# Kernel optimization log

Hardware: AMD Instinct MI355X
Metric: run time of the kernel (lower is better)

The kernel has to match this reference:

```python
import jax, jax.numpy as jnp
import numpy as np

IN_CH = 256
BOT = IN_CH // 2  # bottleneck channels
B, W, H = 4, 64, 64


def setup_inputs() -> dict:
    key = jax.random.key(0)
    ks = jax.random.split(key, 10)
    s_in = 1.0 / np.sqrt(IN_CH)   # torch Conv2d default init scale (kaiming-ish bound)
    s_bt = 1.0 / np.sqrt(BOT)
    return {
        "X": jax.random.normal(ks[0], (B, IN_CH, W, H), dtype=jnp.float32),
        "Wq": jax.random.uniform(ks[1], (BOT, IN_CH), jnp.float32, -s_in, s_in),
        "bq": jax.random.uniform(ks[2], (BOT,), jnp.float32, -s_in, s_in),
        "Wk": jax.random.uniform(ks[3], (BOT, IN_CH), jnp.float32, -s_in, s_in),
        "bk": jax.random.uniform(ks[4], (BOT,), jnp.float32, -s_in, s_in),
        "Wv": jax.random.uniform(ks[5], (BOT, IN_CH), jnp.float32, -s_in, s_in),
        "bv": jax.random.uniform(ks[6], (BOT,), jnp.float32, -s_in, s_in),
        "Wo": jax.random.uniform(ks[7], (IN_CH, BOT), jnp.float32, -s_bt, s_bt),
        "bo": jax.random.uniform(ks[8], (IN_CH,), jnp.float32, -s_bt, s_bt),
        "gamma": 0.1 * jax.random.normal(ks[9], (1,), dtype=jnp.float32),
    }


def reference(X, Wq, bq, Wk, bk, Wv, bv, Wo, bo, gamma):
    b, c, w, h = X.shape
    n = w * h
    Xf = X.reshape(b, c, n)  # [b, c, n] — 1x1 conv == per-pixel linear
    q = jnp.einsum('oc,bcn->bon', Wq, Xf) + bq[None, :, None]  # [b, c/2, n]
    k = jnp.einsum('oc,bcn->bon', Wk, Xf) + bk[None, :, None]
    v = jnp.einsum('oc,bcn->bon', Wv, Xf) + bv[None, :, None]
    # score[b,i,j] = sum_c q[b,c,i] * k[b,c,j]; softmax over dim=1 (query index i)
    score = jnp.einsum('bci,bcj->bij', q, k)          # [b, n, n]
    attn = jax.nn.softmax(score, axis=1)
    out = jnp.einsum('bci,bij->bcj', v, attn)         # [b, c/2, n]
    out = jnp.einsum('oc,bcn->bon', Wo, out) + bo[None, :, None]  # [b, c, n]
    out = out.reshape(b, c, w, h)
    return gamma[0] * out + X
```

## Files before the change

### kernel.cpp

```cpp
#include <hip/hip_runtime.h>
#include <math.h>

#define NBATCH 4
#define CIN    256
#define CBOT   128
#define NPIX   4096
#define NPART  4
#define LOG2E  1.44269504f

typedef __attribute__((ext_vector_type(4))) float f32x4;
typedef __attribute__((ext_vector_type(8))) short bf16x8;

__device__ __forceinline__ unsigned short f2bf(float f) {
    union { float f; unsigned u; } v; v.f = f;
    unsigned r = (v.u + 0x7FFFu + ((v.u >> 16) & 1u)) >> 16;
    return (unsigned short)r;
}
__device__ __forceinline__ unsigned pk2bf(float a, float b) {
#if __has_builtin(__builtin_amdgcn_cvt_pk_bf16_f32)
    auto r = __builtin_amdgcn_cvt_pk_bf16_f32(a, b);
    unsigned u; __builtin_memcpy(&u, &r, 4); return u;
#else
    return (unsigned)f2bf(a) | ((unsigned)f2bf(b) << 16);
#endif
}
__device__ __forceinline__ float fexp2(float x) {
#if __has_builtin(__builtin_amdgcn_exp2f)
    return __builtin_amdgcn_exp2f(x);
#else
    return exp2f(x);
#endif
}
__device__ __forceinline__ void plswap32(unsigned &a, unsigned &b) {
#if __has_builtin(__builtin_amdgcn_permlane32_swap)
    auto r = __builtin_amdgcn_permlane32_swap(a, b, false, false);
    a = (unsigned)r[0]; b = (unsigned)r[1];
#else
    asm volatile("v_permlane32_swap_b32 %0, %1" : "+v"(a), "+v"(b));
#endif
}
__device__ __forceinline__ void plswap16(unsigned &a, unsigned &b) {
#if __has_builtin(__builtin_amdgcn_permlane16_swap)
    auto r = __builtin_amdgcn_permlane16_swap(a, b, false, false);
    a = (unsigned)r[0]; b = (unsigned)r[1];
#else
    asm volatile("v_permlane16_swap_b32 %0, %1" : "+v"(a), "+v"(b));
#endif
}

__global__ __launch_bounds__(256) void k_wcvt(
    const float* __restrict__ Wq, const float* __restrict__ Wk,
    const float* __restrict__ Wv, const float* __restrict__ Wo,
    unsigned short* __restrict__ Wb)
{
    const int f4 = (blockIdx.x * 256 + threadIdx.x) * 4;
    const int reg = f4 >> 15, loc = f4 & 32767;
    const float* __restrict__ W = (reg == 0) ? Wq : (reg == 1) ? Wk : (reg == 2) ? Wv : Wo;
    const float sc = (reg == 1) ? LOG2E : 1.f;
    float4 v = *(const float4*)(W + loc);
    uint2 u;
    u.x = pk2bf(v.x * sc, v.y * sc);
    u.y = pk2bf(v.z * sc, v.w * sc);
    *(uint2*)&Wb[f4] = u;
}

__global__ __launch_bounds__(256) void k_qkvx(
    const float* __restrict__ X,
    const unsigned short* __restrict__ Wb,
    const float* __restrict__ bq, const float* __restrict__ bk,
    const float* __restrict__ bv,
    unsigned short* __restrict__ Qt, unsigned short* __restrict__ Kt,
    unsigned short* __restrict__ Vt)
{
    __shared__ __align__(16) unsigned short Xs[32][264];
    const int tid = threadIdx.x;
    const int wv = tid >> 6, lane = tid & 63;
    const int grp = lane & 15, quad = lane >> 4;
    const int pbase = blockIdx.x * 32;
    const int b     = blockIdx.y;
    const float* __restrict__ Xg = X + (size_t)b * CIN * NPIX + pbase;

#pragma unroll
    for (int k = 0; k < 8; ++k) {
        int f = tid + 256 * k;
        int c = f >> 3, pg = (f & 7) << 2;
        float4 v = *(const float4*)(Xg + (size_t)c * NPIX + pg);
        Xs[pg + 0][c] = f2bf(v.x);
        Xs[pg + 1][c] = f2bf(v.y);
        Xs[pg + 2][c] = f2bf(v.z);
        Xs[pg + 3][c] = f2bf(v.w);
    }
    __syncthreads();

    const unsigned short* __restrict__ Wqb = Wb;
    const unsigned short* __restrict__ Wkb = Wb + 32768;
    const unsigned short* __restrict__ Wvb = Wb + 65536;
    const int obase = 32 * wv;

    f32x4 aQ[2][2], aK[2][2], aV[2][2];
#pragma unroll
    for (int mt = 0; mt < 2; ++mt)
#pragma unroll
        for (int nt = 0; nt < 2; ++nt) {
            aQ[mt][nt] = (f32x4)0.f; aK[mt][nt] = (f32x4)0.f; aV[mt][nt] = (f32x4)0.f;
        }

    for (int ks = 0; ks < 8; ++ks) {
        bf16x8 bx[2];
#pragma unroll
        for (int nt = 0; nt < 2; ++nt)
            bx[nt] = *(const bf16x8*)&Xs[nt * 16 + grp][ks * 32 + quad * 8];
        bf16x8 wq_[2], wk_[2], wv_[2];
#pragma unroll
        for (int mt = 0; mt < 2; ++mt) {
            const size_t roff = (size_t)(obase + mt * 16 + grp) * CIN + ks * 32 + quad * 8;
            wq_[mt] = *(const bf16x8*)&Wqb[roff];
            wk_[mt] = *(const bf16x8*)&Wkb[roff];
            wv_[mt] = *(const bf16x8*)&Wvb[roff];
        }
#pragma unroll
        for (int mt = 0; mt < 2; ++mt)
#pragma unroll
            for (int nt = 0; nt < 2; ++nt) {
                aQ[mt][nt] = __builtin_amdgcn_mfma_f32_16x16x32_bf16(wq_[mt], bx[nt], aQ[mt][nt], 0, 0, 0);
                aK[mt][nt] = __builtin_amdgcn_mfma_f32_16x16x32_bf16(wk_[mt], bx[nt], aK[mt][nt], 0, 0, 0);
                aV[mt][nt] = __builtin_amdgcn_mfma_f32_16x16x32_bf16(bx[mt], wv_[nt], aV[mt][nt], 0, 0, 0);
            }
    }

    unsigned short* Qb_ = Qt + (size_t)b * NPIX * CBOT;
    unsigned short* Kb_ = Kt + (size_t)b * NPIX * CBOT;
#pragma unroll
    for (int mt = 0; mt < 2; ++mt) {
        int o0 = obase + mt * 16 + quad * 4;
        float b4q[4], b4k[4];
#pragma unroll
        for (int r = 0; r < 4; ++r) { b4q[r] = bq[o0 + r]; b4k[r] = bk[o0 + r] * LOG2E; }
#pragma unroll
        for (int nt = 0; nt < 2; ++nt) {
            int p = pbase + nt * 16 + grp;
            uint2 uq, uk;
            uq.x = pk2bf(aQ[mt][nt][0] + b4q[0], aQ[mt][nt][1] + b4q[1]);
            uq.y = pk2bf(aQ[mt][nt][2] + b4q[2], aQ[mt][nt][3] + b4q[3]);
            uk.x = pk2bf(aK[mt][nt][0] + b4k[0], aK[mt][nt][1] + b4k[1]);
            uk.y = pk2bf(aK[mt][nt][2] + b4k[2], aK[mt][nt][3] + b4k[3]);
            *(uint2*)&Qb_[(size_t)p * CBOT + o0] = uq;
            *(uint2*)&Kb_[(size_t)p * CBOT + o0] = uk;
        }
    }
    unsigned short* Vb_ = Vt + (size_t)b * CBOT * NPIX;
#pragma unroll
    for (int nt = 0; nt < 2; ++nt) {
        int o = obase + nt * 16 + grp;
        float bb = bv[o];
#pragma unroll
        for (int mt = 0; mt < 2; ++mt) {
            int p0 = pbase + mt * 16 + quad * 4;
            uint2 u;
            u.x = pk2bf(aV[mt][nt][0] + bb, aV[mt][nt][1] + bb);
            u.y = pk2bf(aV[mt][nt][2] + bb, aV[mt][nt][3] + bb);
            *(uint2*)&Vb_[(size_t)o * NPIX + p0] = u;
        }
    }
}

__global__ __launch_bounds__(256, 2) void k_flash(
    const unsigned short* __restrict__ Qt,
    const unsigned short* __restrict__ Kt,
    const unsigned short* __restrict__ Vt,
    unsigned short* __restrict__ Opart,
    float* __restrict__ Lpart)
{
    extern __shared__ __align__(16) unsigned short lds[];
#define QS(bi, r, c) lds[(bi) * 8704 + (r) * 136 + (c)]
#define VS(bi, r, c) lds[17408 + (bi) * 9216 + (r) * 72 + (c)]
    const int tid  = threadIdx.x;
    const int wv   = tid >> 6, lane = tid & 63;
    const int grp  = lane & 15, quad = lane >> 4;
    const int jblk = blockIdx.x * 128;
    const int part = blockIdx.y;
    const int b    = blockIdx.z;
    const int tbeg = part * (64 / NPART);
    const int tend = tbeg + (64 / NPART);
    const unsigned short* __restrict__ Qb = Qt + (size_t)b * NPIX * CBOT;
    const unsigned short* __restrict__ Kb = Kt + (size_t)b * NPIX * CBOT;
    const unsigned short* __restrict__ Vb = Vt + (size_t)b * CBOT * NPIX;

    bf16x8 bk[2][4];
#pragma unroll
    for (int nt = 0; nt < 2; ++nt)
#pragma unroll
        for (int ks = 0; ks < 4; ++ks)
            bk[nt][ks] = *(const bf16x8*)&Kb[
                (size_t)(jblk + wv * 32 + nt * 16 + grp) * CBOT + ks * 32 + quad * 8];

    bf16x8 aones;
#pragma unroll
    for (int t = 0; t < 8; ++t) aones[t] = (short)0x3F80;

    f32x4 o[8][2];
#pragma unroll
    for (int ct = 0; ct < 8; ++ct) { o[ct][0] = (f32x4)0.f; o[ct][1] = (f32x4)0.f; }
    f32x4 lacc[2] = {(f32x4)0.f, (f32x4)0.f};

    const int qrow = tid >> 4, qch = tid & 15;
    const int vrow = tid >> 3, vch = tid & 7;
    bf16x8 qreg[4], vreg[4];
#pragma unroll
    for (int k = 0; k < 4; ++k) {
        qreg[k] = *(const bf16x8*)&Qb[(size_t)(tbeg * 64 + qrow + 16 * k) * CBOT + qch * 8];
        vreg[k] = *(const bf16x8*)&Vb[(size_t)(vrow + 32 * k) * NPIX + tbeg * 64 + vch * 8];
    }
#pragma unroll
    for (int k = 0; k < 4; ++k) {
        *(bf16x8*)&QS(0, qrow + 16 * k, qch * 8) = qreg[k];
        *(bf16x8*)&VS(0, vrow + 32 * k, vch * 8) = vreg[k];
    }
    {
        const int i1 = (tbeg + 1) * 64;
#pragma unroll
        for (int k = 0; k < 4; ++k) {
            qreg[k] = *(const bf16x8*)&Qb[(size_t)(i1 + qrow + 16 * k) * CBOT + qch * 8];
            vreg[k] = *(const bf16x8*)&Vb[(size_t)(vrow + 32 * k) * NPIX + i1 + vch * 8];
        }
    }
    __syncthreads();

    for (int it = tbeg; it < tend; ++it) {
        const int cur = (it - tbeg) & 1;

        f32x4 sf[4][2];
#pragma unroll
        for (int mt = 0; mt < 4; ++mt) { sf[mt][0] = (f32x4)0.f; sf[mt][1] = (f32x4)0.f; }
#pragma unroll
        for (int mt = 0; mt < 4; ++mt)
#pragma unroll
            for (int ks = 0; ks < 4; ++ks) {
                bf16x8 aq_ = *(const bf16x8*)&QS(cur, mt * 16 + grp, ks * 32 + quad * 8);
                sf[mt][0] = __builtin_amdgcn_mfma_f32_16x16x32_bf16(aq_, bk[0][ks], sf[mt][0], 0, 0, 0);
                sf[mt][1] = __builtin_amdgcn_mfma_f32_16x16x32_bf16(aq_, bk[1][ks], sf[mt][1], 0, 0, 0);
            }

        if (it + 1 < tend) {
#pragma unroll
            for (int k = 0; k < 4; ++k) {
                *(bf16x8*)&QS(cur ^ 1, qrow + 16 * k, qch * 8) = qreg[k];
                *(bf16x8*)&VS(cur ^ 1, vrow + 32 * k, vch * 8) = vreg[k];
            }
            if (it + 2 < tend) {
                const int i2 = (it + 2) * 64;
#pragma unroll
                for (int k = 0; k < 4; ++k) {
                    qreg[k] = *(const bf16x8*)&Qb[(size_t)(i2 + qrow + 16 * k) * CBOT + qch * 8];
                    vreg[k] = *(const bf16x8*)&Vb[(size_t)(vrow + 32 * k) * NPIX + i2 + vch * 8];
                }
            }
        }

        bf16x8 pf[2][2];
#pragma unroll
        for (int nt = 0; nt < 2; ++nt)
#pragma unroll
            for (int h = 0; h < 2; ++h) {
                unsigned u0a = pk2bf(fexp2(sf[2 * h][nt][0]),     fexp2(sf[2 * h][nt][1]));
                unsigned u1a = pk2bf(fexp2(sf[2 * h][nt][2]),     fexp2(sf[2 * h][nt][3]));
                unsigned u0b = pk2bf(fexp2(sf[2 * h + 1][nt][0]), fexp2(sf[2 * h + 1][nt][1]));
                unsigned u1b = pk2bf(fexp2(sf[2 * h + 1][nt][2]), fexp2(sf[2 * h + 1][nt][3]));
                plswap32(u0a, u0b); plswap16(u0a, u0b);
                plswap32(u1a, u1b); plswap16(u1a, u1b);
                union { unsigned u[4]; bf16x8 v; } cvt;
                cvt.u[0] = u0a; cvt.u[1] = u1a; cvt.u[2] = u0b; cvt.u[3] = u1b;
                pf[nt][h] = cvt.v;
            }

#pragma unroll
        for (int ct = 0; ct < 8; ++ct)
#pragma unroll
            for (int h = 0; h < 2; ++h) {
                bf16x8 av_ = *(const bf16x8*)&VS(cur, ct * 16 + grp, h * 32 + quad * 8);
                o[ct][0] = __builtin_amdgcn_mfma_f32_16x16x32_bf16(av_, pf[0][h], o[ct][0], 0, 0, 0);
                o[ct][1] = __builtin_amdgcn_mfma_f32_16x16x32_bf16(av_, pf[1][h], o[ct][1], 0, 0, 0);
            }
#pragma unroll
        for (int nt = 0; nt < 2; ++nt) {
            lacc[nt] = __builtin_amdgcn_mfma_f32_16x16x32_bf16(aones, pf[nt][0], lacc[nt], 0, 0, 0);
            lacc[nt] = __builtin_amdgcn_mfma_f32_16x16x32_bf16(aones, pf[nt][1], lacc[nt], 0, 0, 0);
        }

        if (it + 1 < tend) __syncthreads();
    }

    unsigned short* Ob = Opart + ((size_t)(part * NBATCH + b) * NPIX + jblk) * CBOT;
#pragma unroll
    for (int nt = 0; nt < 2; ++nt) {
        const size_t jrow = (size_t)(wv * 32 + nt * 16 + grp) * CBOT;
#pragma unroll
        for (int ct = 0; ct < 8; ++ct) {
            uint2 u;
            u.x = pk2bf(o[ct][nt][0], o[ct][nt][1]);
            u.y = pk2bf(o[ct][nt][2], o[ct][nt][3]);
            *(uint2*)&Ob[jrow + ct * 16 + quad * 4] = u;
        }
    }
    if (quad == 0) {
#pragma unroll
        for (int nt = 0; nt < 2; ++nt)
            Lpart[(size_t)(part * NBATCH + b) * NPIX + jblk + wv * 32 + nt * 16 + grp] =
                lacc[nt][0];
    }
#undef QS
#undef VS
}

__global__ __launch_bounds__(256) void k_oproj(
    const unsigned short* __restrict__ Opart, const float* __restrict__ Lpart,
    const unsigned short* __restrict__ Wob, const float* __restrict__ bo,
    const float* __restrict__ gamma, const float* __restrict__ X,
    float* __restrict__ Out)
{
    const int tid = threadIdx.x;
    const int wv = tid >> 6, lane = tid & 63;
    const int grp = lane & 15, quad = lane >> 4;
    const int pbase = blockIdx.x * 32;
    const int b     = blockIdx.y;
    const int obase = 64 * wv;

    f32x4 acc[2][4];
#pragma unroll
    for (int mt = 0; mt < 2; ++mt)
#pragma unroll
        for (int nt = 0; nt < 4; ++nt) acc[mt][nt] = (f32x4)0.f;

    for (int ks = 0; ks < 4; ++ks) {
        bf16x8 bw[4];
#pragma unroll
        for (int nt = 0; nt < 4; ++nt)
            bw[nt] = *(const bf16x8*)&Wob[(size_t)(obase + nt * 16 + grp) * CBOT + ks * 32 + quad * 8];
#pragma unroll
        for (int mt = 0; mt < 2; ++mt) {
            int p = pbase + mt * 16 + grp;
#pragma unroll
            for (int part = 0; part < NPART; ++part) {
                bf16x8 ao = *(const bf16x8*)&Opart[
                    ((size_t)(part * NBATCH + b) * NPIX + p) * CBOT + ks * 32 + quad * 8];
#pragma unroll
                for (int nt = 0; nt < 4; ++nt)
                    acc[mt][nt] = __builtin_amdgcn_mfma_f32_16x16x32_bf16(ao, bw[nt], acc[mt][nt], 0, 0, 0);
            }
        }
    }

    float linv[2][4];
#pragma unroll
    for (int mt = 0; mt < 2; ++mt)
#pragma unroll
        for (int r = 0; r < 4; ++r) {
            int p = pbase + mt * 16 + quad * 4 + r;
            float ls = 0.f;
#pragma unroll
            for (int part = 0; part < NPART; ++part)
                ls += Lpart[(size_t)(part * NBATCH + b) * NPIX + p];
            linv[mt][r] = 1.f / ls;
        }
    float g = gamma[0];
#pragma unroll
    for (int nt = 0; nt < 4; ++nt) {
        int o = obase + nt * 16 + grp;
        float bb = bo[o];
#pragma unroll
        for (int mt = 0; mt < 2; ++mt) {
            int p0 = pbase + mt * 16 + quad * 4;
            size_t base = (size_t)b * CIN * NPIX + (size_t)o * NPIX + p0;
            float4 x4 = *(const float4*)(X + base);
            float4 r4;
            r4.x = g * (acc[mt][nt][0] * linv[mt][0] + bb) + x4.x;
            r4.y = g * (acc[mt][nt][1] * linv[mt][1] + bb) + x4.y;
            r4.z = g * (acc[mt][nt][2] * linv[mt][2] + bb) + x4.z;
            r4.w = g * (acc[mt][nt][3] * linv[mt][3] + bb) + x4.w;
            *(float4*)(Out + base) = r4;
        }
    }
}

extern "C" void kernel_launch(void* const* d_in, const int* in_sizes, int n_in,
                              void* d_out, int out_size, void* d_ws, size_t ws_size,
                              hipStream_t stream)
{
    (void)in_sizes; (void)n_in; (void)out_size; (void)ws_size;
    const float* X     = (const float*)d_in[0];
    const float* Wq    = (const float*)d_in[1];
    const float* bq    = (const float*)d_in[2];
    const float* Wk    = (const float*)d_in[3];
    const float* bk    = (const float*)d_in[4];
    const float* Wv    = (const float*)d_in[5];
    const float* bv    = (const float*)d_in[6];
    const float* Wo    = (const float*)d_in[7];
    const float* bo    = (const float*)d_in[8];
    const float* gamma = (const float*)d_in[9];
    float* out = (float*)d_out;

    const size_t BNC = (size_t)NBATCH * NPIX * CBOT;
    unsigned short* Qt    = (unsigned short*)d_ws;
    unsigned short* Kt    = Qt + BNC;
    unsigned short* Vt    = Kt + BNC;
    unsigned short* Opart = Vt + BNC;
    float*          Lpart = (float*)(Opart + (size_t)NPART * BNC);
    unsigned short* Wb    = (unsigned short*)(Lpart + (size_t)NPART * NBATCH * NPIX);

    const int flash_lds = 2 * (64 * 136 + 128 * 72) * 2;

    k_wcvt <<<dim3(128),               256, 0,         stream>>>(Wq, Wk, Wv, Wo, Wb);
    k_qkvx <<<dim3(128, NBATCH),       256, 0,         stream>>>(X, Wb, bq, bk, bv, Qt, Kt, Vt);
    k_flash<<<dim3(32, NPART, NBATCH), 256, flash_lds, stream>>>(Qt, Kt, Vt, Opart, Lpart);
    k_oproj<<<dim3(128, NBATCH),       256, 0,         stream>>>(Opart, Lpart, Wb + 98304, bo, gamma, X, out);
}
```

Baseline: 162.0 us.

## Read Q and V tiles directly from global memory and remap flash block order

The flash-attention kernel drops its double-buffered LDS staging of Q and V tiles and its per-iteration barriers. Each wave now loads MFMA operands straight from global memory, relying on L1/L2 caching. The block index is also remapped so that blocks running at the same time share batch and partition data, which aims to improve L2 locality. This removes LDS traffic and synchronisation, but every wave now fetches the same Q/V data redundantly with higher-latency global loads and no software prefetch.

New measurement: 259.7 us. 60.3% more time.

```diff
diff --git a/kernel.cpp b/kernel.cpp
--- a/kernel.cpp
+++ b/kernel.cpp
@@ -164,24 +164,26 @@
     }
 }
 
-__global__ __launch_bounds__(256, 2) void k_flash(
+__global__ __launch_bounds__(256) void k_flash(
     const unsigned short* __restrict__ Qt,
     const unsigned short* __restrict__ Kt,
     const unsigned short* __restrict__ Vt,
     unsigned short* __restrict__ Opart,
     float* __restrict__ Lpart)
 {
-    extern __shared__ __align__(16) unsigned short lds[];
-#define QS(bi, r, c) lds[(bi) * 8704 + (r) * 136 + (c)]
-#define VS(bi, r, c) lds[17408 + (bi) * 9216 + (r) * 72 + (c)]
     const int tid  = threadIdx.x;
     const int wv   = tid >> 6, lane = tid & 63;
     const int grp  = lane & 15, quad = lane >> 4;
-    const int jblk = blockIdx.x * 128;
-    const int part = blockIdx.y;
-    const int b    = blockIdx.z;
-    const int tbeg = part * (64 / NPART);
-    const int tend = tbeg + (64 / NPART);
+
+    const int xr    = blockIdx.x;
+    const int pbRaw = blockIdx.y * NBATCH + blockIdx.z;
+    const int jp    = (xr >> 3) + 4 * (pbRaw >> 1);
+    const int pbN   = (xr & 7) * 2 + (pbRaw & 1);
+    const int part  = pbN >> 2;
+    const int b     = pbN & 3;
+    const int jblk  = jp * 128;
+    const int tbeg  = part * (64 / NPART);
+    const int tend  = tbeg + (64 / NPART);
     const unsigned short* __restrict__ Qb = Qt + (size_t)b * NPIX * CBOT;
     const unsigned short* __restrict__ Kb = Kt + (size_t)b * NPIX * CBOT;
     const unsigned short* __restrict__ Vb = Vt + (size_t)b * CBOT * NPIX;
@@ -203,31 +205,8 @@
     for (int ct = 0; ct < 8; ++ct) { o[ct][0] = (f32x4)0.f; o[ct][1] = (f32x4)0.f; }
     f32x4 lacc[2] = {(f32x4)0.f, (f32x4)0.f};
 
-    const int qrow = tid >> 4, qch = tid & 15;
-    const int vrow = tid >> 3, vch = tid & 7;
-    bf16x8 qreg[4], vreg[4];
-#pragma unroll
-    for (int k = 0; k < 4; ++k) {
-        qreg[k] = *(const bf16x8*)&Qb[(size_t)(tbeg * 64 + qrow + 16 * k) * CBOT + qch * 8];
-        vreg[k] = *(const bf16x8*)&Vb[(size_t)(vrow + 32 * k) * NPIX + tbeg * 64 + vch * 8];
-    }
-#pragma unroll
-    for (int k = 0; k < 4; ++k) {
-        *(bf16x8*)&QS(0, qrow + 16 * k, qch * 8) = qreg[k];
-        *(bf16x8*)&VS(0, vrow + 32 * k, vch * 8) = vreg[k];
-    }
-    {
-        const int i1 = (tbeg + 1) * 64;
-#pragma unroll
-        for (int k = 0; k < 4; ++k) {
-            qreg[k] = *(const bf16x8*)&Qb[(size_t)(i1 + qrow + 16 * k) * CBOT + qch * 8];
-            vreg[k] = *(const bf16x8*)&Vb[(size_t)(vrow + 32 * k) * NPIX + i1 + vch * 8];
-        }
-    }
-    __syncthreads();
-
     for (int it = tbeg; it < tend; ++it) {
-        const int cur = (it - tbeg) & 1;
+        const size_t i0 = (size_t)it * 64;
 
         f32x4 sf[4][2];
 #pragma unroll
@@ -236,26 +215,11 @@
         for (int mt = 0; mt < 4; ++mt)
 #pragma unroll
             for (int ks = 0; ks < 4; ++ks) {
-                bf16x8 aq_ = *(const bf16x8*)&QS(cur, mt * 16 + grp, ks * 32 + quad * 8);
+                bf16x8 aq_ = *(const bf16x8*)&Qb[
+                    (i0 + mt * 16 + grp) * CBOT + ks * 32 + quad * 8];
                 sf[mt][0] = __builtin_amdgcn_mfma_f32_16x16x32_bf16(aq_, bk[0][ks], sf[mt][0], 0, 0, 0);
                 sf[mt][1] = __builtin_amdgcn_mfma_f32_16x16x32_bf16(aq_, bk[1][ks], sf[mt][1], 0, 0, 0);
             }
-
-        if (it + 1 < tend) {
-#pragma unroll
-            for (int k = 0; k < 4; ++k) {
-                *(bf16x8*)&QS(cur ^ 1, qrow + 16 * k, qch * 8) = qreg[k];
-                *(bf16x8*)&VS(cur ^ 1, vrow + 32 * k, vch * 8) = vreg[k];
-            }
-            if (it + 2 < tend) {
-                const int i2 = (it + 2) * 64;
-#pragma unroll
-                for (int k = 0; k < 4; ++k) {
-                    qreg[k] = *(const bf16x8*)&Qb[(size_t)(i2 + qrow + 16 * k) * CBOT + qch * 8];
-                    vreg[k] = *(const bf16x8*)&Vb[(size_t)(vrow + 32 * k) * NPIX + i2 + vch * 8];
-                }
-            }
-        }
 
         bf16x8 pf[2][2];
 #pragma unroll
@@ -277,7 +241,8 @@
         for (int ct = 0; ct < 8; ++ct)
 #pragma unroll
             for (int h = 0; h < 2; ++h) {
-                bf16x8 av_ = *(const bf16x8*)&VS(cur, ct * 16 + grp, h * 32 + quad * 8);
+                bf16x8 av_ = *(const bf16x8*)&Vb[
+                    (size_t)(ct * 16 + grp) * NPIX + i0 + h * 32 + quad * 8];
                 o[ct][0] = __builtin_amdgcn_mfma_f32_16x16x32_bf16(av_, pf[0][h], o[ct][0], 0, 0, 0);
                 o[ct][1] = __builtin_amdgcn_mfma_f32_16x16x32_bf16(av_, pf[1][h], o[ct][1], 0, 0, 0);
             }
@@ -286,11 +251,9 @@
             lacc[nt] = __builtin_amdgcn_mfma_f32_16x16x32_bf16(aones, pf[nt][0], lacc[nt], 0, 0, 0);
             lacc[nt] = __builtin_amdgcn_mfma_f32_16x16x32_bf16(aones, pf[nt][1], lacc[nt], 0, 0, 0);
         }
-
-        if (it + 1 < tend) __syncthreads();
-    }
-
-    unsigned short* Ob = Opart + ((size_t)(part * NBATCH + b) * NPIX + jblk) * CBOT;
+    }
+
+    unsigned short* Ob = Opart + ((size_t)pbN * NPIX + jblk) * CBOT;
 #pragma unroll
     for (int nt = 0; nt < 2; ++nt) {
         const size_t jrow = (size_t)(wv * 32 + nt * 16 + grp) * CBOT;
@@ -305,11 +268,9 @@
     if (quad == 0) {
 #pragma unroll
         for (int nt = 0; nt < 2; ++nt)
-            Lpart[(size_t)(part * NBATCH + b) * NPIX + jblk + wv * 32 + nt * 16 + grp] =
+            Lpart[(size_t)pbN * NPIX + jblk + wv * 32 + nt * 16 + grp] =
                 lacc[nt][0];
     }
-#undef QS
-#undef VS
 }
 
 __global__ __launch_bounds__(256) void k_oproj(
@@ -407,10 +368,8 @@
     float*          Lpart = (float*)(Opart + (size_t)NPART * BNC);
     unsigned short* Wb    = (unsigned short*)(Lpart + (size_t)NPART * NBATCH * NPIX);
 
-    const int flash_lds = 2 * (64 * 136 + 128 * 72) * 2;
-
-    k_wcvt <<<dim3(128),               256, 0,         stream>>>(Wq, Wk, Wv, Wo, Wb);
-    k_qkvx <<<dim3(128, NBATCH),       256, 0,         stream>>>(X, Wb, bq, bk, bv, Qt, Kt, Vt);
-    k_flash<<<dim3(32, NPART, NBATCH), 256, flash_lds, stream>>>(Qt, Kt, Vt, Opart, Lpart);
-    k_oproj<<<dim3(128, NBATCH),       256, 0,         stream>>>(Opart, Lpart, Wb + 98304, bo, gamma, X, out);
-}
+    k_wcvt <<<dim3(128),               256, 0, stream>>>(Wq, Wk, Wv, Wo, Wb);
+    k_qkvx <<<dim3(128, NBATCH),       256, 0, stream>>>(X, Wb, bq, bk, bv, Qt, Kt, Vt);
+    k_flash<<<dim3(32, NPART, NBATCH), 256, 0, stream>>>(Qt, Kt, Vt, Opart, Lpart);
+    k_oproj<<<dim3(128, NBATCH),       256, 0, stream>>>(Opart, Lpart, Wb + 98304, bo, gamma, X, out);
+}
```
